# Kernel tuning notes

Hardware: AMD Instinct MI355X
Metric: run time of the kernel (lower is better)

## Reference

```python
import jax, jax.numpy as jnp
import numpy as np

B, H, W = 8, 128, 128
WIDTH, MODES = 32, 12
NL = 6


def _spectral_conv(x, w):
    # x: [B,C,H,W] real; w: [2, Cin, Cout, m, m, 2] (real/imag packed)
    b, c, h, ww = x.shape
    m = w.shape[3]
    xf = jnp.fft.rfft2(x)  # [B,C,H,W//2+1] complex
    w1 = w[0, ..., 0] + 1j * w[0, ..., 1]
    w2 = w[1, ..., 0] + 1j * w[1, ..., 1]
    top = jnp.einsum('bixy,ioxy->boxy', xf[:, :, :m, :m], w1)
    bot = jnp.einsum('bixy,ioxy->boxy', xf[:, :, -m:, :m], w2)
    out = jnp.zeros((b, w.shape[2], h, ww // 2 + 1), dtype=xf.dtype)
    out = out.at[:, :, :m, :m].set(top).at[:, :, -m:, :m].set(bot)
    return jnp.fft.irfft2(out, s=(h, ww))


def _conv1x1(x, wgt, bia):
    # x: [B,C,H,W], wgt: [O,C], bia: [O]
    return jnp.einsum('bchw,oc->bohw', x, wgt) + bia[None, :, None, None]


def _gelu(x):
    return jax.nn.gelu(x, approximate=False)


def setup_inputs() -> dict:
    key = jax.random.key(0)
    ks = jax.random.split(key, 20)
    scale = 1.0 / (WIDTH * WIDTH)
    d = {}
    d['x'] = jax.random.normal(ks[0], (B, H, W, 4), jnp.float32)
    d['fc0_W'] = jax.random.normal(ks[1], (4, WIDTH), jnp.float32) * 0.5
    d['fc0_b'] = jnp.zeros((WIDTH,), jnp.float32)
    d['spec_w'] = scale * jax.random.uniform(ks[2], (NL, 2, WIDTH, WIDTH, MODES, MODES, 2), jnp.float32)
    d['wW'] = jax.random.normal(ks[3], (NL, WIDTH, WIDTH), jnp.float32) * (1.0 / np.sqrt(WIDTH))
    d['wb'] = jnp.zeros((NL, WIDTH), jnp.float32)
    d['bW'] = jax.random.normal(ks[4], (NL, WIDTH, 2), jnp.float32) * 0.7
    d['bb'] = jnp.zeros((NL, WIDTH), jnp.float32)
    d['cW'] = jax.random.normal(ks[5], (NL, WIDTH, 3), jnp.float32) * 0.57
    d['cb'] = jnp.zeros((NL, WIDTH), jnp.float32)
    d['fc1_W'] = jax.random.normal(ks[6], (WIDTH, 256), jnp.float32) * (1.0 / np.sqrt(WIDTH))
    d['fc1_b'] = jnp.zeros((256,), jnp.float32)
    d['fc3_W'] = jax.random.normal(ks[7], (256, 128), jnp.float32) * (1.0 / 16.0)
    d['fc3_b'] = jnp.zeros((128,), jnp.float32)
    d['fc4_W'] = jax.random.normal(ks[8], (128, 128), jnp.float32) * (1.0 / np.sqrt(128.0))
    d['fc4_b'] = jnp.zeros((128,), jnp.float32)
    d['fc5_W'] = jax.random.normal(ks[9], (128, 1), jnp.float32) * (1.0 / np.sqrt(128.0))
    d['fc5_b'] = jnp.zeros((1,), jnp.float32)
    return d


def reference(x, fc0_W, fc0_b, spec_w, wW, wb, bW, bb, cW, cb,
              fc1_W, fc1_b, fc3_W, fc3_b, fc4_W, fc4_b, fc5_W, fc5_b):
    b, h, w, _ = x.shape
    grid_mesh = jnp.transpose(x[:, :, :, 1:4], (0, 3, 1, 2))  # [B,3,H,W]
    y = x @ fc0_W + fc0_b                                     # [B,H,W,width]
    y = jnp.transpose(y, (0, 3, 1, 2))                        # [B,width,H,W]
    gx = jnp.linspace(0.0, 1.0, h, dtype=jnp.float32)
    gy = jnp.linspace(0.0, 1.0, w, dtype=jnp.float32)
    grid = jnp.stack([
        jnp.broadcast_to(gx[:, None], (h, w)),
        jnp.broadcast_to(gy[None, :], (h, w)),
    ], axis=0)                                                # [2,H,W]
    grid = jnp.broadcast_to(grid[None], (b, 2, h, w))
    for l in range(NL):
        y = _gelu(_spectral_conv(y, spec_w[l])
                  + _conv1x1(y, wW[l], wb[l])
                  + _conv1x1(grid, bW[l], bb[l])
                  + _conv1x1(grid_mesh, cW[l], cb[l]))
    y = jnp.transpose(y, (0, 2, 3, 1))                        # [B,H,W,width]
    y = _gelu(y @ fc1_W + fc1_b)
    y = _gelu(y @ fc3_W + fc3_b)
    y = y @ fc4_W + fc4_b
    y = y @ fc5_W + fc5_b
    return y
```

## Files before the change

### kernel.cpp

```cpp
#include <hip/hip_runtime.h>
#include <math.h>


#define NL 6

typedef unsigned short u16;
typedef __attribute__((ext_vector_type(8))) short short8v;
typedef __attribute__((ext_vector_type(8))) unsigned short ushort8v;
typedef __attribute__((ext_vector_type(4))) unsigned short ushort4v;
typedef __attribute__((ext_vector_type(4))) float f32x4;

__device__ __forceinline__ float gelu_f(float x){
  float z  = x*0.70710678118654752f;
  float az = fabsf(z);
  float t  = __builtin_amdgcn_rcpf(fmaf(0.3275911f, az, 1.0f));
  float p  = t*(0.254829592f + t*(-0.284496736f + t*(1.421413741f +
             t*(-1.453152027f + t*1.061405429f))));
  float e  = __expf(-z*z);
  float er = copysignf(fmaf(-p, e, 1.0f), z);
  return 0.5f*x*(1.0f + er);
}
__device__ __forceinline__ u16 f2bf(float x){
  unsigned u = __float_as_uint(x);
  u += 0x7FFF + ((u>>16)&1);
  return (u16)(u>>16);
}
__device__ __forceinline__ float bf2f(u16 h){
  return __uint_as_float(((unsigned)h)<<16);
}
__device__ __forceinline__ void split2(float v, u16 &hh, u16 &ll){
  unsigned u = __float_as_uint(v);
  hh = (u16)(u>>16);
  float lo = v - __uint_as_float(u & 0xFFFF0000u);
  ll = (u16)(__float_as_uint(lo)>>16);
}

__global__ __launch_bounds__(256) void k_fc0f(const float* __restrict__ x,
                      const float* __restrict__ W, const float* __restrict__ b,
                      u16* __restrict__ Ybh, u16* __restrict__ Ybl,
                      float* __restrict__ F1){
  __shared__ float Ws[128];
  __shared__ float bs[32];
  __shared__ float ys2[2][32][132];
  int t = threadIdx.x;
  if (t < 128) Ws[t] = W[t];
  if (t < 32)  bs[t] = b[t];
  __syncthreads();
  int pix = blockIdx.x*256 + t;
  float4 xv = *reinterpret_cast<const float4*>(x + (size_t)pix*4);
  int r = t>>7, w = t&127;
  ushort8v hv[4], lv[4];
  #pragma unroll
  for (int c=0;c<32;c++){
    float acc = bs[c] + xv.x*Ws[c] + xv.y*Ws[32+c] + xv.z*Ws[64+c] + xv.w*Ws[96+c];
    ys2[r][c][w] = acc;
    u16 hh, ll; split2(acc, hh, ll);
    hv[c>>3][c&7] = hh; lv[c>>3][c&7] = ll;
  }
  {
    u16* dh = Ybh + (size_t)pix*32;
    u16* dl = Ybl + (size_t)pix*32;
    #pragma unroll
    for (int q=0;q<4;q++){
      *reinterpret_cast<ushort8v*>(dh + q*8) = hv[q];
      *reinterpret_cast<ushort8v*>(dl + q*8) = lv[q];
    }
  }
  __syncthreads();
  int c2 = t>>3, wq = t&7;
  float stc[12], sts[12];
  #pragma unroll
  for (int k=0;k<12;k++){ float s,c; sincospif(k*(1.0f/64.0f), &s, &c); stc[k]=c; sts[k]=s; }
  int gr0 = blockIdx.x*2;
  #pragma unroll
  for (int r2=0;r2<2;r2++){
    float cr[12], ci[12], aR[12], aI[12];
    #pragma unroll
    for (int k=0;k<12;k++){
      float s,c; sincospif((float)(k*wq)*0.25f, &s, &c);
      cr[k]=c; ci[k]=s; aR[k]=0.f; aI[k]=0.f;
    }
    const float* rowp = &ys2[r2][c2][wq*16];
    #pragma unroll
    for (int q=0;q<4;q++){
      float4 xq = *reinterpret_cast<const float4*>(rowp + q*4);
      float xa[4]={xq.x,xq.y,xq.z,xq.w};
      #pragma unroll
      for (int e=0;e<4;e++){
        float xw = xa[e];
        #pragma unroll
        for (int k=0;k<12;k++){
          aR[k] += xw*cr[k];
          aI[k] -= xw*ci[k];
          float nc = cr[k]*stc[k] - ci[k]*sts[k];
          ci[k]    = cr[k]*sts[k] + ci[k]*stc[k];
          cr[k] = nc;
        }
      }
    }
    #pragma unroll
    for (int k=0;k<12;k++){
      aR[k] += __shfl_xor(aR[k],1); aR[k] += __shfl_xor(aR[k],2); aR[k] += __shfl_xor(aR[k],4);
      aI[k] += __shfl_xor(aI[k],1); aI[k] += __shfl_xor(aI[k],2); aI[k] += __shfl_xor(aI[k],4);
    }
    if (wq==0){
      int g = gr0 + r2; int b2 = g>>7, h2 = g&127;
      float* dst = F1 + ((size_t)(b2*32+c2)*128 + h2)*24;
      #pragma unroll
      for (int k=0;k<12;k++){ dst[2*k] = aR[k]; dst[2*k+1] = aI[k]; }
    }
  }
}

__global__ __launch_bounds__(256) void k_wtrans(const float* __restrict__ w, float* __restrict__ wT){
  __shared__ float buf[16][32][25];
  int t=threadIdx.x;
  int beta = blockIdx.x;
  int l = beta/48, r = beta%48;
  int hf = r/24; int r2 = r%24;
  int kym = r2>>1; int i0 = (r2&1)*16;
  const float* src = w + (size_t)l*589824 + (size_t)hf*294912 + kym*24;
  float* dst = wT + (size_t)l*589824 + (size_t)hf*294912 + (size_t)kym*24576;
  for (int j=t; j<12288; j+=256){
    int i = j/768, rem = j%768, o = rem/24, kxri = rem%24;
    buf[i][o][kxri] = src[(size_t)(i0+i)*9216 + o*288 + kxri];
  }
  __syncthreads();
  for (int j=t; j<12288; j+=256){
    int kx = j>>10, rem = j&1023, i = rem>>6, orr = rem&63, o = orr>>1, ri = orr&1;
    dst[(size_t)kx*2048 + o*64 + (i0+i)*2 + ri] = buf[i][o][kx*2+ri];
  }
}

__global__ __launch_bounds__(256) void k_wprep(const float* __restrict__ W1, const float* __restrict__ W3,
                       const float* __restrict__ W4,
                       const float* __restrict__ b4, const float* __restrict__ w5,
                       const float* __restrict__ b5,
                       const float* __restrict__ wW, const float* __restrict__ wb,
                       const float* __restrict__ bb, const float* __restrict__ cb,
                       u16* __restrict__ W1h, u16* __restrict__ W1l,
                       u16* __restrict__ W3h, u16* __restrict__ W3l,
                       u16* __restrict__ W4h, u16* __restrict__ W4l,
                       u16* __restrict__ Emh, u16* __restrict__ Eml,
                       u16* __restrict__ E2h, u16* __restrict__ E2l,
                       u16* __restrict__ E3h, u16* __restrict__ E3l,
                       u16* __restrict__ Wch, u16* __restrict__ Wcl,
                       u16* __restrict__ E4h, u16* __restrict__ E4l,
                       float* __restrict__ bsum, float* __restrict__ c45){
  __shared__ float buf[32][132];
  int t = threadIdx.x, bid = blockIdx.x;
  if (bid < 8){
    int k0 = bid*32;
    for (int i=t;i<4096;i+=256){ int k=i>>7, n=i&127; buf[k][n] = W3[(size_t)(k0+k)*128 + n]; }
    __syncthreads();
    int n = t>>1, kq = t&1;
    #pragma unroll
    for (int kk=0;kk<16;kk++){
      int k = kq*16 + kk;
      float v = buf[k][n];
      u16 hh = f2bf(v);
      W3h[(size_t)bid*4096 + n*32 + k] = hh;
      W3l[(size_t)bid*4096 + n*32 + k] = f2bf(v - bf2f(hh));
    }
  } else if (bid == 8){
    __shared__ float red[256];
    int n = t;
    #pragma unroll
    for (int c=0;c<32;c++){
      float v = W1[(size_t)c*256 + n];
      u16 hh = f2bf(v);
      W1h[n*32 + c] = hh;
      W1l[n*32 + c] = f2bf(v - bf2f(hh));
    }
    red[t] = (t<128)? b4[t]*w5[t] : 0.f;
    __syncthreads();
    for (int s2=128; s2>0; s2>>=1){
      if (t<s2) red[t] += red[t+s2];
      __syncthreads();
    }
    if (t==0) c45[0] = red[0] + b5[0];
  } else if (bid <= 12){
    int k0 = (bid-9)*32;
    for (int i=t;i<4096;i+=256){ int k=i>>7, n=i&127; buf[k][n] = W4[(size_t)(k0+k)*128 + n]; }
    __syncthreads();
    int n = t>>1, kq = t&1;
    #pragma unroll
    for (int kk=0;kk<16;kk++){
      int k = kq*16 + kk;
      float v = buf[k][n];
      u16 hh = f2bf(v);
      W4h[(size_t)(bid-9)*4096 + n*32 + k] = hh;
      W4l[(size_t)(bid-9)*4096 + n*32 + k] = f2bf(v - bf2f(hh));
    }
  } else if (bid == 13){
    for (int i=t;i<4096;i+=256){
      int m=i>>7, w=i&127;
      float v=0.f;
      if (m<24){ float s,c; sincospif((float)((m>>1)*w)*(1.0f/64.0f), &s, &c); v = (m&1)? -s : c; }
      u16 hh, ll; split2(v, hh, ll);
      Emh[i]=hh; Eml[i]=ll;
    }
  } else if (bid == 14){
    for (int i=t;i<12288;i+=256){
      int m=i>>8, k=i&255;
      int kyi = (m<24)? m : m-24;
      int ky  = (kyi<12)? kyi : kyi+104;
      int h   = k&127;
      int mm  = (ky*h)&127;
      float s,c; sincospif((float)mm*(1.0f/64.0f), &s, &c);
      bool sinSlot = k>=128;
      float v;
      if (m<24) v = sinSlot? s : c;
      else      v = sinSlot? c : -s;
      u16 hh, ll; split2(v, hh, ll);
      E2h[i]=hh; E2l[i]=ll;
    }
  } else if (bid == 15){
    for (int i=t;i<8192;i+=256){
      int h=i>>6, k=i&63;
      float v=0.f;
      if (k<48){
        int kyi = (k<24)? k : k-24;
        int ky  = (kyi<12)? kyi : kyi+104;
        int mm  = (ky*h)&127;
        float s,c; sincospif((float)mm*(1.0f/64.0f), &s, &c);
        v = ((k<24)? c : s) * (1.0f/16384.0f);
      }
      u16 hh, ll; split2(v, hh, ll);
      E3h[i]=hh; E3l[i]=ll;
    }
  } else if (bid == 16){
    for (int i=t;i<6144;i+=256){
      float v = wW[i];
      u16 hh, ll; split2(v, hh, ll);
      Wch[i]=hh; Wcl[i]=ll;
    }
    if (t < 192) bsum[t] = wb[t] + bb[t] + cb[t];
  } else {
    for (int i=t;i<4096;i+=256){
      int w=i>>5, k=i&31;
      float v=0.f;
      if (k < 24){
        int kx = k>>1, ri = k&1;
        if (kx==0) v = ri? 0.f : 1.f;
        else {
          float s,c; sincospif((float)(kx*w)*(1.0f/64.0f), &s, &c);
          v = ri? -2.f*s : 2.f*c;
        }
      }
      u16 hh, ll; split2(v, hh, ll);
      E4h[i]=hh; E4l[i]=ll;
    }
  }
}

__global__ __launch_bounds__(256) void k_dfth(const float* __restrict__ F1,
                      const u16* __restrict__ E2h, const u16* __restrict__ E2l,
                      float* __restrict__ F2){
  __shared__ u16 Fth[16*264], Ftl[16*264];
  int t=threadIdx.x;
  int bc = blockIdx.x;
  int b = bc>>5, c = bc&31;
  const float* src = F1 + (size_t)bc*3072;
  for (int i=t;i<3072;i+=256){
    int h = i/24, col = i - h*24;
    int kx = col>>1, ri = col&1;
    u16 hh, ll; split2(src[i], hh, ll);
    int idx = kx*264 + ri*128 + h;
    Fth[idx] = hh; Ftl[idx] = ll;
  }
  __syncthreads();
  int wv = t>>6, lane = t&63, lr = lane&15, lg = lane>>4;
  if (wv < 3){
    f32x4 acc = (f32x4){0.f,0.f,0.f,0.f};
    #pragma unroll
    for (int ks=0; ks<8; ++ks){
      short8v af = *reinterpret_cast<const short8v*>(E2h + (size_t)(wv*16+lr)*256 + ks*32 + lg*8);
      short8v ag = *reinterpret_cast<const short8v*>(E2l + (size_t)(wv*16+lr)*256 + ks*32 + lg*8);
      short8v bf = *reinterpret_cast<const short8v*>(&Fth[lr*264 + ks*32 + lg*8]);
      short8v bg = *reinterpret_cast<const short8v*>(&Ftl[lr*264 + ks*32 + lg*8]);
      acc = __builtin_amdgcn_mfma_f32_16x16x32_bf16(af, bf, acc, 0,0,0);
      acc = __builtin_amdgcn_mfma_f32_16x16x32_bf16(af, bg, acc, 0,0,0);
      acc = __builtin_amdgcn_mfma_f32_16x16x32_bf16(ag, bf, acc, 0,0,0);
    }
    if (lr < 12){
      #pragma unroll
      for (int r=0;r<4;r++){
        int m = wv*16 + 4*lg + r;
        int kyi = (m<24)? m : m-24;
        int ri  = (m<24)? 0 : 1;
        F2[(((size_t)b*24 + kyi)*24 + 2*lr + ri)*32 + c] = acc[r];
      }
    }
  }
}

__global__ __launch_bounds__(576) void k_mixid(const float* __restrict__ F2, const float* __restrict__ wTl,
                      const u16* __restrict__ E3h, const u16* __restrict__ E3l,
                      u16* __restrict__ S1h, u16* __restrict__ S1l){
  __shared__ u16 Bh[32*72], Bl[32*72];
  int t=threadIdx.x;
  int bo = blockIdx.x;
  int b = bo>>5, o = bo&31;
  for (int i=t; i<24*24; i+=576){
    int row = i/24, k = 48 + i - (i/24)*24;
    Bh[row*72 + k] = 0; Bl[row*72 + k] = 0;
  }
  {
    int pair = t>>1, half = t&1;
    int kx = pair%12, kyi = pair/12;
    int hf = kyi<12?0:1, kym = kyi<12?kyi:kyi-12;
    const float* fpr = F2 + (((size_t)b*24 + kyi)*24 + 2*kx)*32 + half*16;
    const float* fpi = fpr + 32;
    const float* wp = wTl + (size_t)(hf*12+kym)*24576 + kx*2048 + o*64 + half*32;
    float gr=0.f, gi=0.f;
    #pragma unroll 8
    for (int i=0;i<16;i++){
      float2 wv = *reinterpret_cast<const float2*>(wp + 2*i);
      float ar = fpr[i], ai = fpi[i];
      gr += ar*wv.x - ai*wv.y;
      gi += ar*wv.y + ai*wv.x;
    }
    gr += __shfl_xor(gr,1);
    gi += __shfl_xor(gi,1);
    if (half==0){
      u16 grh, grl, gih, gil, nih, nil;
      split2(gr, grh, grl);
      split2(gi, gih, gil);
      split2(-gi, nih, nil);
      int r0 = (2*kx)*72, r1 = (2*kx+1)*72;
      Bh[r0 + kyi]      = grh; Bl[r0 + kyi]      = grl;
      Bh[r0 + 24 + kyi] = nih; Bl[r0 + 24 + kyi] = nil;
      Bh[r1 + kyi]      = gih; Bl[r1 + kyi]      = gil;
      Bh[r1 + 24 + kyi] = grh; Bl[r1 + 24 + kyi] = grl;
    }
  }
  __syncthreads();
  int wv = t>>6, lane = t&63, lr = lane&15, lg = lane>>4;
  if (wv < 8){
    f32x4 acc[2];
    acc[0] = (f32x4){0.f,0.f,0.f,0.f};
    acc[1] = (f32x4){0.f,0.f,0.f,0.f};
    #pragma unroll
    for (int ks=0; ks<2; ++ks){
      short8v af = *reinterpret_cast<const short8v*>(E3h + (size_t)(wv*16+lr)*64 + ks*32 + lg*8);
      short8v ag = *reinterpret_cast<const short8v*>(E3l + (size_t)(wv*16+lr)*64 + ks*32 + lg*8);
      #pragma unroll
      for (int nt=0; nt<2; ++nt){
        short8v bf = *reinterpret_cast<const short8v*>(&Bh[(nt*16+lr)*72 + ks*32 + lg*8]);
        short8v bg = *reinterpret_cast<const short8v*>(&Bl[(nt*16+lr)*72 + ks*32 + lg*8]);
        acc[nt] = __builtin_amdgcn_mfma_f32_16x16x32_bf16(af, bf, acc[nt], 0,0,0);
        acc[nt] = __builtin_amdgcn_mfma_f32_16x16x32_bf16(af, bg, acc[nt], 0,0,0);
        acc[nt] = __builtin_amdgcn_mfma_f32_16x16x32_bf16(ag, bf, acc[nt], 0,0,0);
      }
    }
    #pragma unroll
    for (int nt=0; nt<2; ++nt){
      int n = nt*16 + lr;
      if (n < 24){
        #pragma unroll
        for (int r=0;r<4;r++){
          int h = wv*16 + 4*lg + r;
          size_t off = (size_t)bo*3072 + h*24 + n;
          u16 hh, ll; split2(acc[nt][r], hh, ll);
          S1h[off] = hh; S1l[off] = ll;
        }
      }
    }
  }
}

template<int LAST>
__global__ __launch_bounds__(256) void k_combine3(
    const u16* __restrict__ Ybh_in, const u16* __restrict__ Ybl_in,
    const u16* __restrict__ S1h, const u16* __restrict__ S1l,
    const float* __restrict__ x,
    const u16* __restrict__ Wch, const u16* __restrict__ Wcl,
    const u16* __restrict__ E4h, const u16* __restrict__ E4l,
    const float* __restrict__ bsuml,
    const float* __restrict__ bWl, const float* __restrict__ cWl,
    const u16* __restrict__ Emh, const u16* __restrict__ Eml,
    float* __restrict__ F1,
    u16* __restrict__ Ybh_out, u16* __restrict__ Ybl_out){
  __shared__ u16 ybsp[2][32][136];
  __shared__ float bs[32], bwS[64], cwS[96];
  int t=threadIdx.x;
  int b = blockIdx.x>>7, h = blockIdx.x&127;
  if (t<32) bs[t]=bsuml[t];
  else if (t>=64 && t<128) bwS[t-64]=bWl[t-64];
  else if (t>=128 && t<224) cwS[t-128]=cWl[t-128];
  __syncthreads();
  int wv=t>>6, lane=t&63, lr=lane&15, lg=lane>>4;
  f32x4 acc[2][2];
  #pragma unroll
  for (int ot=0;ot<2;++ot){ acc[ot][0]=(f32x4){0,0,0,0}; acc[ot][1]=(f32x4){0,0,0,0}; }
  #pragma unroll
  for (int ot=0; ot<2; ++ot){
    int o = ot*16+lr;
    short8v af = *reinterpret_cast<const short8v*>(Wch + o*32 + lg*8);
    short8v al = *reinterpret_cast<const short8v*>(Wcl + o*32 + lg*8);
    #pragma unroll
    for (int j=0;j<2;++j){
      int w = (2*wv+j)*16 + lr;
      size_t yoff = (((size_t)(b*128+h))*128 + w)*32 + lg*8;
      short8v bh = *reinterpret_cast<const short8v*>(Ybh_in + yoff);
      short8v bl = *reinterpret_cast<const short8v*>(Ybl_in + yoff);
      acc[ot][j] = __builtin_amdgcn_mfma_f32_16x16x32_bf16(af, bh, acc[ot][j], 0,0,0);
      acc[ot][j] = __builtin_amdgcn_mfma_f32_16x16x32_bf16(af, bl, acc[ot][j], 0,0,0);
      acc[ot][j] = __builtin_amdgcn_mfma_f32_16x16x32_bf16(al, bh, acc[ot][j], 0,0,0);
    }
  }
  #pragma unroll
  for (int ot=0; ot<2; ++ot){
    int o = ot*16+lr;
    size_t soff = (((size_t)(b*32+o))*128 + h)*24 + lg*8;
    short8v ah = *reinterpret_cast<const short8v*>(S1h + soff);
    short8v al2 = *reinterpret_cast<const short8v*>(S1l + soff);
    #pragma unroll
    for (int j=0;j<2;++j){
      int w = (2*wv+j)*16 + lr;
      short8v eh = *reinterpret_cast<const short8v*>(E4h + w*32 + lg*8);
      short8v el = *reinterpret_cast<const short8v*>(E4l + w*32 + lg*8);
      acc[ot][j] = __builtin_amdgcn_mfma_f32_16x16x32_bf16(ah, eh, acc[ot][j], 0,0,0);
      acc[ot][j] = __builtin_amdgcn_mfma_f32_16x16x32_bf16(al2, eh, acc[ot][j], 0,0,0);
      acc[ot][j] = __builtin_amdgcn_mfma_f32_16x16x32_bf16(ah, el, acc[ot][j], 0,0,0);
    }
  }
  float gx = h*(1.0f/127.0f);
  #pragma unroll
  for (int j=0;j<2;++j){
    int w = (2*wv+j)*16 + lr;
    float4 xm = *reinterpret_cast<const float4*>(x + (((size_t)(b*128+h))*128+w)*4);
    float gy = w*(1.0f/127.0f);
    #pragma unroll
    for (int ot=0;ot<2;++ot){
      ushort4v hv, lvv;
      #pragma unroll
      for (int r=0;r<4;++r){
        int o = ot*16 + 4*lg + r;
        float v = acc[ot][j][r] + bs[o] + gx*bwS[2*o] + gy*bwS[2*o+1]
                + xm.y*cwS[3*o] + xm.z*cwS[3*o+1] + xm.w*cwS[3*o+2];
        float g = gelu_f(v);
        u16 hh, ll; split2(g, hh, ll);
        hv[r]=hh; lvv[r]=ll;
        if constexpr(!LAST){ ybsp[0][o][w]=hh; ybsp[1][o][w]=ll; }
      }
      size_t base = (((size_t)(b*128+h))*128 + w)*32 + ot*16 + 4*lg;
      *reinterpret_cast<ushort4v*>(Ybh_out + base) = hv;
      *reinterpret_cast<ushort4v*>(Ybl_out + base) = lvv;
    }
  }
  if constexpr(!LAST){
    __syncthreads();
    int mt = wv&1, oj = wv>>1;
    f32x4 accm = (f32x4){0.f,0.f,0.f,0.f};
    #pragma unroll
    for (int ks=0; ks<4; ++ks){
      short8v ef = *reinterpret_cast<const short8v*>(Emh + (size_t)(mt*16+lr)*128 + ks*32 + lg*8);
      short8v eg = *reinterpret_cast<const short8v*>(Eml + (size_t)(mt*16+lr)*128 + ks*32 + lg*8);
      short8v yf = *reinterpret_cast<const short8v*>(&ybsp[0][oj*16+lr][ks*32+lg*8]);
      short8v yg = *reinterpret_cast<const short8v*>(&ybsp[1][oj*16+lr][ks*32+lg*8]);
      accm = __builtin_amdgcn_mfma_f32_16x16x32_bf16(ef, yf, accm, 0,0,0);
      accm = __builtin_amdgcn_mfma_f32_16x16x32_bf16(ef, yg, accm, 0,0,0);
      accm = __builtin_amdgcn_mfma_f32_16x16x32_bf16(eg, yf, accm, 0,0,0);
    }
    if (mt==0 || lg<2){
      int m = mt*16 + 4*lg;
      int o = oj*16 + lr;
      float4 v; v.x=accm[0]; v.y=accm[1]; v.z=accm[2]; v.w=accm[3];
      *reinterpret_cast<float4*>(&F1[((size_t)(b*32+o)*128 + h)*24 + m]) = v;
    }
  }
}

__global__ __launch_bounds__(256) void k_headm(
    const u16* __restrict__ Yb,
    const u16* __restrict__ W1h, const u16* __restrict__ W1l,
    const float* __restrict__ b1,
    const u16* __restrict__ W3h, const u16* __restrict__ W3l,
    const float* __restrict__ b3,
    const u16* __restrict__ W4h, const u16* __restrict__ W4l,
    const float* __restrict__ c45, const float* __restrict__ w5,
    float* __restrict__ out){
  __shared__ u16 Ac[64*264];
  __shared__ float b1s[256];
  __shared__ float b3s[128], w5s[128];
  __shared__ float part2[2][64];
  int t = threadIdx.x;
  int wv = t>>6, lane = t&63, lr = lane&15, lg = lane>>4;
  int P0 = blockIdx.x*64;
  b1s[t] = b1[t];
  if (t<128){ b3s[t]=b3[t]; w5s[t]=w5[t]; }
  int wn3 = wv>>1, wp = wv&1;
  short8v yb;
  {
    size_t p = (size_t)P0 + wv*16 + lr;
    yb = *reinterpret_cast<const short8v*>(Yb + p*32 + lg*8);
  }
  __syncthreads();
  unsigned q[8][2][2];
  #pragma unroll
  for (int kt=0; kt<8; ++kt){
    f32x4 a1[2];
    a1[0]=(f32x4){0,0,0,0}; a1[1]=(f32x4){0,0,0,0};
    #pragma unroll
    for (int i=0;i<2;i++){
      int n1 = kt*32 + i*16 + lr;
      short8v w1f = *reinterpret_cast<const short8v*>(W1h + (size_t)n1*32 + lg*8);
      short8v w1g = *reinterpret_cast<const short8v*>(W1l + (size_t)n1*32 + lg*8);
      a1[i] = __builtin_amdgcn_mfma_f32_16x16x32_bf16(w1f, yb, a1[i], 0,0,0);
      a1[i] = __builtin_amdgcn_mfma_f32_16x16x32_bf16(w1g, yb, a1[i], 0,0,0);
    }
    #pragma unroll
    for (int i=0;i<2;i++){
      int n1b = kt*32 + i*16 + 4*lg;
      u16 v0 = f2bf(gelu_f(a1[i][0] + b1s[n1b+0]));
      u16 v1 = f2bf(gelu_f(a1[i][1] + b1s[n1b+1]));
      u16 v2 = f2bf(gelu_f(a1[i][2] + b1s[n1b+2]));
      u16 v3 = f2bf(gelu_f(a1[i][3] + b1s[n1b+3]));
      q[kt][i][0] = (unsigned)v0 | ((unsigned)v1<<16);
      q[kt][i][1] = (unsigned)v2 | ((unsigned)v3<<16);
    }
  }
  {
    int p = wv*16 + lr;
    #pragma unroll
    for (int kt=0; kt<8; ++kt){
      #pragma unroll
      for (int i=0;i<2;i++){
        union { unsigned u[2]; ushort4v s; } cv;
        cv.u[0] = q[kt][i][0]; cv.u[1] = q[kt][i][1];
        *reinterpret_cast<ushort4v*>(&Ac[p*264 + kt*32 + i*16 + 4*lg]) = cv.s;
      }
    }
  }
  __syncthreads();
  f32x4 acc3[4][2];
  #pragma unroll
  for (int i=0;i<4;i++){ acc3[i][0]=(f32x4){0,0,0,0}; acc3[i][1]=(f32x4){0,0,0,0}; }
  #pragma unroll
  for (int kt=0; kt<8; ++kt){
    short8v ab[2];
    #pragma unroll
    for (int j=0;j<2;j++){
      int pb = wp*32 + j*16 + lr;
      ab[j] = *reinterpret_cast<const short8v*>(&Ac[pb*264 + kt*32 + lg*8]);
    }
    #pragma unroll
    for (int i=0;i<4;i++){
      int n3 = wn3*64 + i*16 + lr;
      short8v w3f = *reinterpret_cast<const short8v*>(W3h + (size_t)kt*4096 + n3*32 + lg*8);
      short8v w3g = *reinterpret_cast<const short8v*>(W3l + (size_t)kt*4096 + n3*32 + lg*8);
      #pragma unroll
      for (int j=0;j<2;j++){
        acc3[i][j] = __builtin_amdgcn_mfma_f32_16x16x32_bf16(w3f, ab[j], acc3[i][j], 0,0,0);
        acc3[i][j] = __builtin_amdgcn_mfma_f32_16x16x32_bf16(w3g, ab[j], acc3[i][j], 0,0,0);
      }
    }
  }
  __syncthreads();
  u16* A2 = Ac;
  #pragma unroll
  for (int i=0;i<4;i++){
    int n3b = wn3*64 + i*16 + 4*lg;
    #pragma unroll
    for (int j=0;j<2;j++){
      int p = wp*32 + j*16 + lr;
      ushort4v hv;
      #pragma unroll
      for (int r=0;r<4;r++){
        hv[r] = f2bf(gelu_f(acc3[i][j][r] + b3s[n3b+r]));
      }
      *reinterpret_cast<ushort4v*>(&A2[p*136 + n3b]) = hv;
    }
  }
  __syncthreads();
  f32x4 acc4[4][2];
  #pragma unroll
  for (int i=0;i<4;i++){ acc4[i][0]=(f32x4){0,0,0,0}; acc4[i][1]=(f32x4){0,0,0,0}; }
  #pragma unroll
  for (int ks=0; ks<4; ++ks){
    short8v p2[2];
    #pragma unroll
    for (int j=0;j<2;j++){
      int p = wp*32 + j*16 + lr;
      p2[j] = *reinterpret_cast<const short8v*>(&A2[p*136 + ks*32 + lg*8]);
    }
    #pragma unroll
    for (int i2=0;i2<4;i2++){
      int n4 = wn3*64 + i2*16 + lr;
      short8v w4f = *reinterpret_cast<const short8v*>(W4h + (size_t)ks*4096 + n4*32 + lg*8);
      short8v w4g = *reinterpret_cast<const short8v*>(W4l + (size_t)ks*4096 + n4*32 + lg*8);
      #pragma unroll
      for (int j=0;j<2;j++){
        acc4[i2][j] = __builtin_amdgcn_mfma_f32_16x16x32_bf16(w4f, p2[j], acc4[i2][j], 0,0,0);
        acc4[i2][j] = __builtin_amdgcn_mfma_f32_16x16x32_bf16(w4g, p2[j], acc4[i2][j], 0,0,0);
      }
    }
  }
  #pragma unroll
  for (int j=0;j<2;j++){
    float part = 0.f;
    #pragma unroll
    for (int i2=0;i2<4;i2++){
      #pragma unroll
      for (int r=0;r<4;r++){
        int n4 = wn3*64 + i2*16 + 4*lg + r;
        part += acc4[i2][j][r] * w5s[n4];
      }
    }
    part += __shfl_xor(part, 16); part += __shfl_xor(part, 32);
    if (lg==0) part2[wn3][wp*32 + j*16 + lr] = part;
  }
  __syncthreads();
  if (t<64) out[P0 + t] = part2[0][t] + part2[1][t] + c45[0];
}

extern "C" void kernel_launch(void* const* d_in, const int* in_sizes, int n_in,
                              void* d_out, int out_size, void* d_ws, size_t ws_size,
                              hipStream_t stream){
  const float* x     = (const float*)d_in[0];
  const float* fc0_W = (const float*)d_in[1];
  const float* fc0_b = (const float*)d_in[2];
  const float* spec_w= (const float*)d_in[3];
  const float* wW    = (const float*)d_in[4];
  const float* wb    = (const float*)d_in[5];
  const float* bW    = (const float*)d_in[6];
  const float* bb    = (const float*)d_in[7];
  const float* cW    = (const float*)d_in[8];
  const float* cb    = (const float*)d_in[9];
  const float* fc1_W = (const float*)d_in[10];
  const float* fc1_b = (const float*)d_in[11];
  const float* fc3_W = (const float*)d_in[12];
  const float* fc3_b = (const float*)d_in[13];
  const float* fc4_W = (const float*)d_in[14];
  const float* fc4_b = (const float*)d_in[15];
  const float* fc5_W = (const float*)d_in[16];
  const float* fc5_b = (const float*)d_in[17];
  float* out = (float*)d_out;
  float* ws  = (float*)d_ws;

  u16*   YbA  = (u16*)ws;
  u16*   YbB  = YbA + 8388608;
  float* wT   = ws + 8388608;
  float* F2   = wT + 3538944;
  u16*   S1h  = (u16*)(F2 + 147456);
  u16*   S1l  = S1h + 786496;
  float* F1   = (float*)(S1l + 786496);
  float* WP   = F1 + 786432;
  u16*   W1h = (u16*)WP;
  u16*   W1l = W1h + 8192;
  u16*   W3h = W1l + 8192;
  u16*   W3l = W3h + 32768;
  u16*   W4h = W3l + 32768;
  u16*   W4l = W4h + 16384;
  u16*   Emh = W4l + 16384;
  u16*   Eml = Emh + 4096;
  u16*   E2h = Eml + 4096;
  u16*   E2l = E2h + 12288;
  u16*   E3h = E2l + 12288;
  u16*   E3l = E3h + 8192;
  u16*   Wch = E3l + 8192;
  u16*   Wcl = Wch + 6144;
  u16*   E4h = Wcl + 6144;
  u16*   E4l = E4h + 4096;
  float* bsum = (float*)(E4l + 4096);
  float* c45  = bsum + 192;
  u16*   YbhA = YbA;
  u16*   YblA = YbA + 4194304;
  u16*   YbhB = YbB;
  u16*   YblB = YbB + 4194304;

  k_fc0f<<<512,256,0,stream>>>(x, fc0_W, fc0_b, YbhA, YblA, F1);
  k_wtrans<<<288,256,0,stream>>>(spec_w, wT);
  k_wprep<<<18,256,0,stream>>>(fc1_W, fc3_W, fc4_W, fc4_b, fc5_W, fc5_b,
                               wW, wb, bb, cb,
                               W1h, W1l, W3h, W3l, W4h, W4l, Emh, Eml,
                               E2h, E2l, E3h, E3l, Wch, Wcl, E4h, E4l,
                               bsum, c45);

  for (int l=0;l<NL;l++){
    const u16* Yih = (l&1)? YbhB : YbhA;
    const u16* Yil = (l&1)? YblB : YblA;
    u16* Yoh = (l&1)? YbhA : YbhB;
    u16* Yol = (l&1)? YblA : YblB;
    k_dfth<<<256,256,0,stream>>>(F1, E2h, E2l, F2);
    k_mixid<<<256,576,0,stream>>>(F2, wT + (size_t)l*589824, E3h, E3l, S1h, S1l);
    if (l < NL-1){
      k_combine3<0><<<1024,256,0,stream>>>(Yih, Yil, S1h, S1l, x,
                                     Wch + l*1024, Wcl + l*1024, E4h, E4l,
                                     bsum + l*32, bW + (size_t)l*64, cW + (size_t)l*96,
                                     Emh, Eml, F1, Yoh, Yol);
    } else {
      k_combine3<1><<<1024,256,0,stream>>>(Yih, Yil, S1h, S1l, x,
                                     Wch + l*1024, Wcl + l*1024, E4h, E4l,
                                     bsum + l*32, bW + (size_t)l*64, cW + (size_t)l*96,
                                     Emh, Eml, nullptr, Yoh, Yol);
    }
  }

  k_headm<<<2048,256,0,stream>>>(YbhA, W1h, W1l, fc1_b, W3h, W3l, fc3_b,
                                 W4h, W4l, c45, fc5_W, out);
}
```

Baseline: 315.0 us.

## Store W-DFT intermediate as pre-split transposed bf16 pairs; halve head LDS buffer

The producers of the W-direction DFT output (fc0 and combine) now split values into bf16 hi/lo and write them directly in the transposed [kx,ri,h] layout. This lets k_dfth read MFMA operands straight from global memory and drop its LDS staging, split pass and barrier. Separately, the head kernel's fc1→fc3 stage is split into two halves so the LDS activation tile shrinks from 264 to 136 columns, which may raise occupancy at the cost of an extra barrier pair. The producer stores become strided 2-byte scatters, which may be less coalesced.

```diff
diff --git a/kernel.cpp b/kernel.cpp
--- a/kernel.cpp
+++ b/kernel.cpp
@@ -38,7 +38,7 @@
 __global__ __launch_bounds__(256) void k_fc0f(const float* __restrict__ x,
                       const float* __restrict__ W, const float* __restrict__ b,
                       u16* __restrict__ Ybh, u16* __restrict__ Ybl,
-                      float* __restrict__ F1){
+                      u16* __restrict__ F1h, u16* __restrict__ F1l){
   __shared__ float Ws[128];
   __shared__ float bs[32];
   __shared__ float ys2[2][32][132];
@@ -105,9 +105,15 @@
     }
     if (wq==0){
       int g = gr0 + r2; int b2 = g>>7, h2 = g&127;
-      float* dst = F1 + ((size_t)(b2*32+c2)*128 + h2)*24;
-      #pragma unroll
-      for (int k=0;k<12;k++){ dst[2*k] = aR[k]; dst[2*k+1] = aI[k]; }
+      size_t base = (size_t)(b2*32+c2)*3072 + h2;
+      #pragma unroll
+      for (int k=0;k<12;k++){
+        u16 hh, ll;
+        split2(aR[k], hh, ll);
+        F1h[base + (2*k)*128]   = hh; F1l[base + (2*k)*128]   = ll;
+        split2(aI[k], hh, ll);
+        F1h[base + (2*k+1)*128] = hh; F1l[base + (2*k+1)*128] = ll;
+      }
     }
   }
 }
@@ -254,31 +260,23 @@
   }
 }
 
-__global__ __launch_bounds__(256) void k_dfth(const float* __restrict__ F1,
+__global__ __launch_bounds__(256) void k_dfth(const u16* __restrict__ F1h, const u16* __restrict__ F1l,
                       const u16* __restrict__ E2h, const u16* __restrict__ E2l,
                       float* __restrict__ F2){
-  __shared__ u16 Fth[16*264], Ftl[16*264];
   int t=threadIdx.x;
   int bc = blockIdx.x;
   int b = bc>>5, c = bc&31;
-  const float* src = F1 + (size_t)bc*3072;
-  for (int i=t;i<3072;i+=256){
-    int h = i/24, col = i - h*24;
-    int kx = col>>1, ri = col&1;
-    u16 hh, ll; split2(src[i], hh, ll);
-    int idx = kx*264 + ri*128 + h;
-    Fth[idx] = hh; Ftl[idx] = ll;
-  }
-  __syncthreads();
   int wv = t>>6, lane = t&63, lr = lane&15, lg = lane>>4;
   if (wv < 3){
+    const u16* bh = F1h + (size_t)bc*3072;
+    const u16* bl = F1l + (size_t)bc*3072;
     f32x4 acc = (f32x4){0.f,0.f,0.f,0.f};
     #pragma unroll
     for (int ks=0; ks<8; ++ks){
       short8v af = *reinterpret_cast<const short8v*>(E2h + (size_t)(wv*16+lr)*256 + ks*32 + lg*8);
       short8v ag = *reinterpret_cast<const short8v*>(E2l + (size_t)(wv*16+lr)*256 + ks*32 + lg*8);
-      short8v bf = *reinterpret_cast<const short8v*>(&Fth[lr*264 + ks*32 + lg*8]);
-      short8v bg = *reinterpret_cast<const short8v*>(&Ftl[lr*264 + ks*32 + lg*8]);
+      short8v bf = *reinterpret_cast<const short8v*>(bh + lr*256 + ks*32 + lg*8);
+      short8v bg = *reinterpret_cast<const short8v*>(bl + lr*256 + ks*32 + lg*8);
       acc = __builtin_amdgcn_mfma_f32_16x16x32_bf16(af, bf, acc, 0,0,0);
       acc = __builtin_amdgcn_mfma_f32_16x16x32_bf16(af, bg, acc, 0,0,0);
       acc = __builtin_amdgcn_mfma_f32_16x16x32_bf16(ag, bf, acc, 0,0,0);
@@ -380,7 +378,7 @@
     const float* __restrict__ bsuml,
     const float* __restrict__ bWl, const float* __restrict__ cWl,
     const u16* __restrict__ Emh, const u16* __restrict__ Eml,
-    float* __restrict__ F1,
+    u16* __restrict__ F1h, u16* __restrict__ F1l,
     u16* __restrict__ Ybh_out, u16* __restrict__ Ybl_out){
   __shared__ u16 ybsp[2][32][136];
   __shared__ float bs[32], bwS[64], cwS[96];
@@ -467,8 +465,13 @@
     if (mt==0 || lg<2){
       int m = mt*16 + 4*lg;
       int o = oj*16 + lr;
-      float4 v; v.x=accm[0]; v.y=accm[1]; v.z=accm[2]; v.w=accm[3];
-      *reinterpret_cast<float4*>(&F1[((size_t)(b*32+o)*128 + h)*24 + m]) = v;
+      size_t base = (size_t)(b*32+o)*3072 + h;
+      #pragma unroll
+      for (int r=0;r<4;++r){
+        u16 hh, ll; split2(accm[r], hh, ll);
+        F1h[base + (m+r)*128] = hh;
+        F1l[base + (m+r)*128] = ll;
+      }
     }
   }
 }
@@ -482,7 +485,7 @@
     const u16* __restrict__ W4h, const u16* __restrict__ W4l,
     const float* __restrict__ c45, const float* __restrict__ w5,
     float* __restrict__ out){
-  __shared__ u16 Ac[64*264];
+  __shared__ u16 Ac[64*136];
   __shared__ float b1s[256];
   __shared__ float b3s[128], w5s[128];
   __shared__ float part2[2][64];
@@ -497,68 +500,74 @@
     size_t p = (size_t)P0 + wv*16 + lr;
     yb = *reinterpret_cast<const short8v*>(Yb + p*32 + lg*8);
   }
+  f32x4 acc3[4][2];
+  #pragma unroll
+  for (int i=0;i<4;i++){ acc3[i][0]=(f32x4){0,0,0,0}; acc3[i][1]=(f32x4){0,0,0,0}; }
   __syncthreads();
-  unsigned q[8][2][2];
-  #pragma unroll
-  for (int kt=0; kt<8; ++kt){
-    f32x4 a1[2];
-    a1[0]=(f32x4){0,0,0,0}; a1[1]=(f32x4){0,0,0,0};
-    #pragma unroll
-    for (int i=0;i<2;i++){
-      int n1 = kt*32 + i*16 + lr;
-      short8v w1f = *reinterpret_cast<const short8v*>(W1h + (size_t)n1*32 + lg*8);
-      short8v w1g = *reinterpret_cast<const short8v*>(W1l + (size_t)n1*32 + lg*8);
-      a1[i] = __builtin_amdgcn_mfma_f32_16x16x32_bf16(w1f, yb, a1[i], 0,0,0);
-      a1[i] = __builtin_amdgcn_mfma_f32_16x16x32_bf16(w1g, yb, a1[i], 0,0,0);
-    }
-    #pragma unroll
-    for (int i=0;i<2;i++){
-      int n1b = kt*32 + i*16 + 4*lg;
-      u16 v0 = f2bf(gelu_f(a1[i][0] + b1s[n1b+0]));
-      u16 v1 = f2bf(gelu_f(a1[i][1] + b1s[n1b+1]));
-      u16 v2 = f2bf(gelu_f(a1[i][2] + b1s[n1b+2]));
-      u16 v3 = f2bf(gelu_f(a1[i][3] + b1s[n1b+3]));
-      q[kt][i][0] = (unsigned)v0 | ((unsigned)v1<<16);
-      q[kt][i][1] = (unsigned)v2 | ((unsigned)v3<<16);
-    }
-  }
-  {
-    int p = wv*16 + lr;
-    #pragma unroll
-    for (int kt=0; kt<8; ++kt){
+
+  #pragma unroll
+  for (int half=0; half<2; ++half){
+    unsigned q[4][2][2];
+    #pragma unroll
+    for (int kq=0; kq<4; ++kq){
+      int kt = half*4 + kq;
+      f32x4 a1[2];
+      a1[0]=(f32x4){0,0,0,0}; a1[1]=(f32x4){0,0,0,0};
       #pragma unroll
       for (int i=0;i<2;i++){
-        union { unsigned u[2]; ushort4v s; } cv;
-        cv.u[0] = q[kt][i][0]; cv.u[1] = q[kt][i][1];
-        *reinterpret_cast<ushort4v*>(&Ac[p*264 + kt*32 + i*16 + 4*lg]) = cv.s;
-      }
-    }
-  }
-  __syncthreads();
-  f32x4 acc3[4][2];
-  #pragma unroll
-  for (int i=0;i<4;i++){ acc3[i][0]=(f32x4){0,0,0,0}; acc3[i][1]=(f32x4){0,0,0,0}; }
-  #pragma unroll
-  for (int kt=0; kt<8; ++kt){
-    short8v ab[2];
-    #pragma unroll
-    for (int j=0;j<2;j++){
-      int pb = wp*32 + j*16 + lr;
-      ab[j] = *reinterpret_cast<const short8v*>(&Ac[pb*264 + kt*32 + lg*8]);
-    }
-    #pragma unroll
-    for (int i=0;i<4;i++){
-      int n3 = wn3*64 + i*16 + lr;
-      short8v w3f = *reinterpret_cast<const short8v*>(W3h + (size_t)kt*4096 + n3*32 + lg*8);
-      short8v w3g = *reinterpret_cast<const short8v*>(W3l + (size_t)kt*4096 + n3*32 + lg*8);
+        int n1 = kt*32 + i*16 + lr;
+        short8v w1f = *reinterpret_cast<const short8v*>(W1h + (size_t)n1*32 + lg*8);
+        short8v w1g = *reinterpret_cast<const short8v*>(W1l + (size_t)n1*32 + lg*8);
+        a1[i] = __builtin_amdgcn_mfma_f32_16x16x32_bf16(w1f, yb, a1[i], 0,0,0);
+        a1[i] = __builtin_amdgcn_mfma_f32_16x16x32_bf16(w1g, yb, a1[i], 0,0,0);
+      }
+      #pragma unroll
+      for (int i=0;i<2;i++){
+        int n1b = kt*32 + i*16 + 4*lg;
+        u16 v0 = f2bf(gelu_f(a1[i][0] + b1s[n1b+0]));
+        u16 v1 = f2bf(gelu_f(a1[i][1] + b1s[n1b+1]));
+        u16 v2 = f2bf(gelu_f(a1[i][2] + b1s[n1b+2]));
+        u16 v3 = f2bf(gelu_f(a1[i][3] + b1s[n1b+3]));
+        q[kq][i][0] = (unsigned)v0 | ((unsigned)v1<<16);
+        q[kq][i][1] = (unsigned)v2 | ((unsigned)v3<<16);
+      }
+    }
+    {
+      int p = wv*16 + lr;
+      #pragma unroll
+      for (int kq=0; kq<4; ++kq){
+        #pragma unroll
+        for (int i=0;i<2;i++){
+          union { unsigned u[2]; ushort4v s; } cv;
+          cv.u[0] = q[kq][i][0]; cv.u[1] = q[kq][i][1];
+          *reinterpret_cast<ushort4v*>(&Ac[p*136 + kq*32 + i*16 + 4*lg]) = cv.s;
+        }
+      }
+    }
+    __syncthreads();
+    #pragma unroll
+    for (int kq=0; kq<4; ++kq){
+      int kt = half*4 + kq;
+      short8v ab[2];
       #pragma unroll
       for (int j=0;j<2;j++){
-        acc3[i][j] = __builtin_amdgcn_mfma_f32_16x16x32_bf16(w3f, ab[j], acc3[i][j], 0,0,0);
-        acc3[i][j] = __builtin_amdgcn_mfma_f32_16x16x32_bf16(w3g, ab[j], acc3[i][j], 0,0,0);
-      }
-    }
-  }
-  __syncthreads();
+        int pb = wp*32 + j*16 + lr;
+        ab[j] = *reinterpret_cast<const short8v*>(&Ac[pb*136 + kq*32 + lg*8]);
+      }
+      #pragma unroll
+      for (int i=0;i<4;i++){
+        int n3 = wn3*64 + i*16 + lr;
+        short8v w3f = *reinterpret_cast<const short8v*>(W3h + (size_t)kt*4096 + n3*32 + lg*8);
+        short8v w3g = *reinterpret_cast<const short8v*>(W3l + (size_t)kt*4096 + n3*32 + lg*8);
+        #pragma unroll
+        for (int j=0;j<2;j++){
+          acc3[i][j] = __builtin_amdgcn_mfma_f32_16x16x32_bf16(w3f, ab[j], acc3[i][j], 0,0,0);
+          acc3[i][j] = __builtin_amdgcn_mfma_f32_16x16x32_bf16(w3g, ab[j], acc3[i][j], 0,0,0);
+        }
+      }
+    }
+    __syncthreads();
+  }
   u16* A2 = Ac;
   #pragma unroll
   for (int i=0;i<4;i++){
@@ -646,8 +655,9 @@
   float* F2   = wT + 3538944;
   u16*   S1h  = (u16*)(F2 + 147456);
   u16*   S1l  = S1h + 786496;
-  float* F1   = (float*)(S1l + 786496);
-  float* WP   = F1 + 786432;
+  u16*   F1h  = S1l + 786496;
+  u16*   F1l  = F1h + 787456;
+  float* WP   = (float*)(F1l + 787456);
   u16*   W1h = (u16*)WP;
   u16*   W1l = W1h + 8192;
   u16*   W3h = W1l + 8192;
@@ -671,7 +681,7 @@
   u16*   YbhB = YbB;
   u16*   YblB = YbB + 4194304;
 
-  k_fc0f<<<512,256,0,stream>>>(x, fc0_W, fc0_b, YbhA, YblA, F1);
+  k_fc0f<<<512,256,0,stream>>>(x, fc0_W, fc0_b, YbhA, YblA, F1h, F1l);
   k_wtrans<<<288,256,0,stream>>>(spec_w, wT);
   k_wprep<<<18,256,0,stream>>>(fc1_W, fc3_W, fc4_W, fc4_b, fc5_W, fc5_b,
                                wW, wb, bb, cb,
@@ -684,18 +694,18 @@
     const u16* Yil = (l&1)? YblB : YblA;
     u16* Yoh = (l&1)? YbhA : YbhB;
     u16* Yol = (l&1)? YblA : YblB;
-    k_dfth<<<256,256,0,stream>>>(F1, E2h, E2l, F2);
+    k_dfth<<<256,256,0,stream>>>(F1h, F1l, E2h, E2l, F2);
     k_mixid<<<256,576,0,stream>>>(F2, wT + (size_t)l*589824, E3h, E3l, S1h, S1l);
     if (l < NL-1){
       k_combine3<0><<<1024,256,0,stream>>>(Yih, Yil, S1h, S1l, x,
                                      Wch + l*1024, Wcl + l*1024, E4h, E4l,
                                      bsum + l*32, bW + (size_t)l*64, cW + (size_t)l*96,
-                                     Emh, Eml, F1, Yoh, Yol);
+                                     Emh, Eml, F1h, F1l, Yoh, Yol);
     } else {
       k_combine3<1><<<1024,256,0,stream>>>(Yih, Yil, S1h, S1l, x,
                                      Wch + l*1024, Wcl + l*1024, E4h, E4l,
                                      bsum + l*32, bW + (size_t)l*64, cW + (size_t)l*96,
-                                     Emh, Eml, nullptr, Yoh, Yol);
+                                     Emh, Eml, nullptr, nullptr, Yoh, Yol);
     }
   }
 
```

New measurement: 339.1 us. 1.08x slower.
